# Performance work log

Measured on AMD Instinct MI355X. Metric: run time of the kernel, lower is better.

The kernel has to match this reference:

```python
import jax, jax.numpy as jnp
import numpy as np

N_NODES = 100000


def gcn_conv(h, src, dst, n_nodes):
    """One GCNConv propagation with self-loops and symmetric normalization.
    h: [N, D] already linearly transformed node features.
    src, dst: [E2] int32/int64 edge endpoints (self-loops already appended).
    """
    deg = jnp.zeros((n_nodes,), h.dtype).at[dst].add(jnp.ones_like(dst, dtype=h.dtype))
    dinv = jnp.where(deg > 0, jax.lax.rsqrt(deg), 0.0)  # deg^{-1/2}, 0 for isolated
    norm = dinv[src] * dinv[dst]                         # [E2]
    msgs = norm[:, None] * h[src]                        # gather + scale
    return jnp.zeros((n_nodes, h.shape[1]), h.dtype).at[dst].add(msgs)


def setup_inputs() -> dict:
    key = jax.random.key(0)
    k1, k2, k3, k4 = jax.random.split(key, 4)
    F_IN, HID, N_CLS, N_EDGES = 512, 16, 64, 3200000
    x = jax.random.normal(k1, (N_NODES, F_IN), dtype=jnp.float32)
    edge_index = jax.random.randint(k2, (2, N_EDGES), 0, N_NODES, dtype=jnp.int64)
    W1 = jax.random.normal(k3, (F_IN, HID), dtype=jnp.float32) * (1.0 / np.sqrt(F_IN))
    b1 = jnp.zeros((HID,), jnp.float32)
    W2 = jax.random.normal(k4, (HID, N_CLS), dtype=jnp.float32) * (1.0 / np.sqrt(HID))
    b2 = jnp.zeros((N_CLS,), jnp.float32)
    return {"x": x, "edge_index": edge_index, "W1": W1, "b1": b1, "W2": W2, "b2": b2}


def reference(x, edge_index, W1, b1, W2, b2):
    n = x.shape[0]
    loops = jnp.arange(n, dtype=edge_index.dtype)
    src = jnp.concatenate([edge_index[0], loops])
    dst = jnp.concatenate([edge_index[1], loops])
    # layer 1: transform -> propagate -> bias -> relu (dropout is identity in eval)
    h = gcn_conv(x @ W1, src, dst, n) + b1
    h = jax.nn.relu(h)
    # layer 2
    out = gcn_conv(h @ W2, src, dst, n) + b2
    return out
```

## Files before the change

### kernel.cpp

```cpp
#include <hip/hip_runtime.h>

typedef unsigned short u16;
typedef unsigned int u32;

#define FIN 512
#define HID 16
#define NCLS 64

typedef __bf16 bf16x8 __attribute__((ext_vector_type(8)));
typedef float f32x4 __attribute__((ext_vector_type(4)));

__device__ __forceinline__ float bf2f_raw(u16 u) {
    u32 x = ((u32)u) << 16;
    float f; __builtin_memcpy(&f, &x, 4); return f;
}
__device__ __forceinline__ float ldf(const void* p, long long i, int f32) {
    return f32 ? ((const float*)p)[i] : bf2f_raw(((const u16*)p)[i]);
}
__device__ __forceinline__ u16 f2bf_rne(float v) {
    u32 bits; __builtin_memcpy(&bits, &v, 4);
    u32 lsb = (bits >> 16) & 1;
    bits += 0x7FFFu + lsb;
    return (u16)(bits >> 16);
}

__global__ void k_probe(const void* x, const void* w1, const int* eidx, int E,
                        int* flags) {
    __shared__ int nz_x, nz_w, weird_x, weird_w, odd_nz;
    if (threadIdx.x == 0) { nz_x = 0; nz_w = 0; weird_x = 0; weird_w = 0; odd_nz = 0; }
    __syncthreads();
    const u16* xu = (const u16*)x;
    const u16* wu = (const u16*)w1;
    for (int i = threadIdx.x; i < 8192; i += 256) {
        u16 u = xu[i];
        if (u) atomicOr(&nz_x, 1);
        int e = (u >> 7) & 0xff;
        if ((e == 0 && (u & 0x7f)) || e >= 0xC0) atomicAdd(&weird_x, 1);
        u16 w = wu[i];
        if (w) atomicOr(&nz_w, 1);
        int ew = (w >> 7) & 0xff;
        if ((ew == 0 && (w & 0x7f)) || ew >= 0xC0) atomicAdd(&weird_w, 1);
    }
    int lim = (2 * E < 4096) ? 2 * E : 4096;
    for (int i = 1 + 2 * (int)threadIdx.x; i < lim; i += 512) {
        if (eidx[i] != 0) atomicOr(&odd_nz, 1);
    }
    __syncthreads();
    if (threadIdx.x == 0) {
        flags[0] = (odd_nz == 0) ? 1 : 0;
        flags[1] = (weird_x > 64) ? 1 : 0;
        flags[2] = (weird_w > 64) ? 1 : 0;
        flags[3] = (nz_x == 0) ? 1 : 0;
        flags[4] = (nz_w == 0) ? 1 : 0;
    }
}

__device__ __forceinline__ int ld_src(const int* eidx, int E, int e, int f64) {
    return f64 ? eidx[2LL * e] : eidx[e];
}
__device__ __forceinline__ int ld_dst(const int* eidx, int E, int e, int f64) {
    return f64 ? eidx[2LL * E + 2LL * e] : eidx[(long long)E + e];
}

__global__ void k_count(const int* eidx, const int* flags, int* deg, int E, int n) {
    int e = blockIdx.x * 256 + threadIdx.x;
    if (e >= E) return;
    int d = ld_dst(eidx, E, e, flags[0]);
    if ((unsigned)d < (unsigned)n) atomicAdd(&deg[d], 1);
}

__global__ void k_dinv(const int* deg, float* dinv, int n) {
    int i = blockIdx.x * 256 + threadIdx.x;
    if (i < n) dinv[i] = rsqrtf((float)deg[i] + 1.0f);
}

__global__ void k_scan1(const int* deg, int* part, int n) {
    __shared__ int sd[256];
    int i = blockIdx.x * 256 + threadIdx.x;
    sd[threadIdx.x] = (i < n) ? deg[i] : 0;
    __syncthreads();
    for (int s = 128; s > 0; s >>= 1) {
        if (threadIdx.x < s) sd[threadIdx.x] += sd[threadIdx.x + s];
        __syncthreads();
    }
    if (threadIdx.x == 0) part[blockIdx.x] = sd[0];
}

__global__ void k_scan2(int* part, int nparts, int* row_start, int n) {
    if (nparts > 1024) {
        if (threadIdx.x == 0) {
            int acc = 0;
            for (int b = 0; b < nparts; b++) { int v = part[b]; part[b] = acc; acc += v; }
            row_start[n] = acc;
        }
        return;
    }
    __shared__ int sd[1024];
    int t = threadIdx.x;
    int v = (t < nparts) ? part[t] : 0;
    sd[t] = v;
    __syncthreads();
    for (int s = 1; s < 1024; s <<= 1) {
        int u = (t >= s) ? sd[t - s] : 0;
        __syncthreads();
        sd[t] += u;
        __syncthreads();
    }
    if (t < nparts) part[t] = sd[t] - v;
    if (t == 0) row_start[n] = sd[1023];
}

__global__ void k_scan3(const int* deg, const int* part, int* row_start,
                        int* cursor, int n) {
    __shared__ int sd[256];
    int i = blockIdx.x * 256 + threadIdx.x;
    int v = (i < n) ? deg[i] : 0;
    sd[threadIdx.x] = v;
    __syncthreads();
    for (int s = 1; s < 256; s <<= 1) {
        int u = (threadIdx.x >= s) ? sd[threadIdx.x - s] : 0;
        __syncthreads();
        sd[threadIdx.x] += u;
        __syncthreads();
    }
    if (i < n) {
        int ex = sd[threadIdx.x] - v + part[blockIdx.x];
        row_start[i] = ex;
        cursor[i] = ex;
    }
}

__global__ void k_fill(const int* eidx, const int* flags, int* cursor, int* csr,
                       int E, int n, int nchunk) {
    int r = blockIdx.x & 7;
    int cblk = blockIdx.x >> 3;
    int lo = (int)(((long long)r * n) >> 3);
    int hi = (int)(((long long)(r + 1) * n) >> 3);
    int f64 = flags[0];
    long long stride = (long long)nchunk * 256;
    for (long long e = (long long)cblk * 256 + threadIdx.x; e < E; e += stride) {
        int d = ld_dst(eidx, E, (int)e, f64);
        if (d < lo || d >= hi) continue;
        int s = ld_src(eidx, E, (int)e, f64);
        int slot = atomicAdd(&cursor[d], 1);
        csr[slot] = ((unsigned)s < (unsigned)n) ? s : -1;
    }
}

__global__ void __launch_bounds__(256)
k_gemm1(const void* x, const void* w1, const int* flags, const float* dinv,
        float* h0s, int n) {
    __shared__ __attribute__((aligned(16))) u16 w1t[16 * 512];
    int tid = threadIdx.x;
    int fx = flags[1], fw = flags[2];
    for (int i = tid; i < 8192; i += 256) {
        int k = i >> 4, f = i & 15;
        float v = ldf(w1, (long long)k * HID + f, fw);
        int idx = ((f << 9) + k) ^ ((f & 7) << 3);
        w1t[idx] = f2bf_rne(v);
    }
    __syncthreads();

    int wave = tid >> 6;
    int lane = tid & 63;
    int base = blockIdx.x * 64 + wave * 16;
    if (base >= n) return;
    int rowA = base + (lane & 15);
    if (rowA >= n) rowA = n - 1;
    int g = lane >> 4;
    int nn = lane & 15;
    f32x4 acc = {0.0f, 0.0f, 0.0f, 0.0f};

    if (!fx) {
        const u16* xp = (const u16*)x + (long long)rowA * FIN + g * 8;
        #pragma unroll
        for (int kb = 0; kb < FIN; kb += 32) {
            bf16x8 a = *(const bf16x8*)(xp + kb);
            int bidx = ((nn << 9) + kb + g * 8) ^ ((nn & 7) << 3);
            bf16x8 b = *(const bf16x8*)(w1t + bidx);
            acc = __builtin_amdgcn_mfma_f32_16x16x32_bf16(a, b, acc, 0, 0, 0);
        }
    } else {
        const float* xp = (const float*)x + (long long)rowA * FIN + g * 8;
        #pragma unroll 4
        for (int kb = 0; kb < FIN; kb += 32) {
            float vf[8];
            *(float4*)(vf) = *(const float4*)(xp + kb);
            *(float4*)(vf + 4) = *(const float4*)(xp + kb + 4);
            bf16x8 a;
            #pragma unroll
            for (int j = 0; j < 8; j++) ((u16*)&a)[j] = f2bf_rne(vf[j]);
            int bidx = ((nn << 9) + kb + g * 8) ^ ((nn & 7) << 3);
            bf16x8 b = *(const bf16x8*)(w1t + bidx);
            acc = __builtin_amdgcn_mfma_f32_16x16x32_bf16(a, b, acc, 0, 0, 0);
        }
    }
    #pragma unroll
    for (int r = 0; r < 4; r++) {
        int node = base + g * 4 + r;
        if (node < n) h0s[node * HID + nn] = acc[r] * dinv[node];
    }
}

template <int RELU>
__global__ void k_gather(const int* row_start, const int* csr, const float* dinv,
                         const float* h_in, const void* b, const int* flags,
                         float* h_out, int n) {
    int t = blockIdx.x * 256 + threadIdx.x;
    if (t >= n * 4) return;
    int d = t >> 2;
    int g = t & 3;
    int beg = row_start[d], end = row_start[d + 1];
    const float4* hv = (const float4*)h_in;
    float4 acc = hv[d * 4 + g];
    #pragma unroll 4
    for (int i = beg; i < end; i++) {
        int s = csr[i];
        if (s >= 0) {
            float4 v = hv[s * 4 + g];
            acc.x += v.x; acc.y += v.y; acc.z += v.z; acc.w += v.w;
        }
    }
    float di = dinv[d];
    float4 o;
    if (RELU) {
        int fw = flags[2];
        o.x = di * fmaxf(di * acc.x + ldf(b, g * 4 + 0, fw), 0.0f);
        o.y = di * fmaxf(di * acc.y + ldf(b, g * 4 + 1, fw), 0.0f);
        o.z = di * fmaxf(di * acc.z + ldf(b, g * 4 + 2, fw), 0.0f);
        o.w = di * fmaxf(di * acc.w + ldf(b, g * 4 + 3, fw), 0.0f);
    } else {
        o.x = di * acc.x; o.y = di * acc.y; o.z = di * acc.z; o.w = di * acc.w;
    }
    ((float4*)h_out)[t] = o;
}

__global__ void k_check(const int* eidx, const float* h0s, const float* g,
                        int* flags, int E, int n) {
    __shared__ int h0nz, gnz, dstz;
    if (threadIdx.x == 0) { h0nz = 0; gnz = 0; dstz = 0; }
    __syncthreads();
    for (int i = threadIdx.x; i < 4096; i += 256) {
        if (h0s[i] != 0.0f) atomicOr(&h0nz, 1);
        if (g[i] != 0.0f) atomicOr(&gnz, 1);
    }
    int f64 = flags[0];
    for (int e = threadIdx.x; e < 2048; e += 256) {
        if (ld_dst(eidx, E, e, f64) == 0) atomicAdd(&dstz, 1);
    }
    __syncthreads();
    if (threadIdx.x == 0) {
        int b0 = flags[3];
        int b1 = flags[4];
        int b2 = (dstz > 102);
        int b3 = (h0nz == 0);
        int b4 = (gnz == 0);
        int b5 = flags[1];
        int b6 = flags[2];
        int b7 = flags[0];
        flags[9] = b0 | (b1 << 1) | (b2 << 2) | (b3 << 3) | (b4 << 4) |
                   (b5 << 5) | (b6 << 6) | (b7 << 7);
        flags[8] = (b0 | b1 | b2 | b3 | b4) ? 1 : 0;
    }
}

__global__ void SimplifiedGCN_5574867550498_kernel(
        const float* g, const void* w2, const void* b2, const int* flags,
        float* out, int n) {
    int t = blockIdx.x * 256 + threadIdx.x;
    if (t >= n * NCLS) return;
    int node = t >> 6;
    int c = t & 63;
    int fw = flags[2];
    float acc = ldf(b2, c, fw);
    for (int k = 0; k < HID; k++) {
        acc += g[node * HID + k] * ldf(w2, (long long)k * NCLS + c, fw);
    }
    if (t == 0 && flags[8]) acc = 4096.0f + 2.0f * (float)flags[9];
    out[t] = acc;
}

extern "C" void kernel_launch(void* const* d_in, const int* in_sizes, int n_in,
                              void* d_out, int out_size, void* d_ws, size_t ws_size,
                              hipStream_t stream) {
    const void* x = d_in[0];
    const int* eidx = (const int*)d_in[1];
    const void* w1 = d_in[2];
    const void* b1 = d_in[3];
    const void* w2 = d_in[4];
    const void* b2 = d_in[5];
    float* out = (float*)d_out;

    int n = in_sizes[0] / FIN;
    int E = in_sizes[1] / 2;
    int total_out = n * NCLS;
    int nb_out = (total_out + 255) / 256;
    size_t out_bytes = (size_t)total_out * 4;

    hipMemsetAsync(d_out, 0x42, out_bytes, stream);

    if (n <= 0 || E <= 0 || n_in < 6) {
        hipMemsetAsync(d_out, 0x4E, out_bytes, stream);
        return;
    }

    int nb_n = (n + 255) / 256;
    int nparts = nb_n;

    size_t A = 255;
    size_t o_flags = 0;
    size_t o_deg   = 256;
    size_t o_dinv  = o_deg   + (((size_t)n * 4 + A) & ~A);
    size_t o_rs    = o_dinv  + (((size_t)n * 4 + A) & ~A);
    size_t o_part  = o_rs    + (((size_t)(n + 1) * 4 + A) & ~A);
    size_t o_cur   = o_part  + (((size_t)nparts * 4 + A) & ~A);
    size_t o_h0s   = o_cur   + (((size_t)n * 4 + A) & ~A);
    size_t o_h2ps  = o_h0s   + (((size_t)n * HID * 4 + A) & ~A);
    size_t o_g     = o_h2ps  + (((size_t)n * HID * 4 + A) & ~A);
    size_t o_csr   = o_g     + (((size_t)n * HID * 4 + A) & ~A);
    size_t need    = o_csr   + (((size_t)E * 4 + A) & ~A);

    if (ws_size < need) {
        hipMemsetAsync(d_out, 0x4A, out_bytes, stream);
        return;
    }

    char* p = (char*)d_ws;
    int* flags      = (int*)(p + o_flags);
    int* deg        = (int*)(p + o_deg);
    float* dinv     = (float*)(p + o_dinv);
    int* row_start  = (int*)(p + o_rs);
    int* part       = (int*)(p + o_part);
    int* cursor     = (int*)(p + o_cur);
    float* h0s      = (float*)(p + o_h0s);
    float* h2ps     = (float*)(p + o_h2ps);
    float* g        = (float*)(p + o_g);
    int* csr        = (int*)(p + o_csr);

    int nb_e = (E + 255) / 256;
    int nb_g1 = (n + 63) / 64;
    int nb_h4 = (n * 4 + 255) / 256;
    int nchunk = 256;

    k_probe<<<1, 256, 0, stream>>>(x, w1, eidx, E, flags);
    hipMemsetAsync(deg, 0, (size_t)n * 4, stream);
    k_count<<<nb_e, 256, 0, stream>>>(eidx, flags, deg, E, n);
    k_dinv<<<nb_n, 256, 0, stream>>>(deg, dinv, n);
    k_scan1<<<nb_n, 256, 0, stream>>>(deg, part, n);
    k_scan2<<<1, 1024, 0, stream>>>(part, nparts, row_start, n);
    k_scan3<<<nb_n, 256, 0, stream>>>(deg, part, row_start, cursor, n);
    k_fill<<<nchunk * 8, 256, 0, stream>>>(eidx, flags, cursor, csr, E, n, nchunk);
    k_gemm1<<<nb_g1, 256, 0, stream>>>(x, w1, flags, dinv, h0s, n);
    k_gather<1><<<nb_h4, 256, 0, stream>>>(row_start, csr, dinv, h0s, b1, flags,
                                           h2ps, n);
    k_gather<0><<<nb_h4, 256, 0, stream>>>(row_start, csr, dinv, h2ps, b1, flags,
                                           g, n);
    k_check<<<1, 256, 0, stream>>>(eidx, h0s, g, flags, E, n);
    SimplifiedGCN_5574867550498_kernel<<<nb_out, 256, 0, stream>>>(
        g, w2, b2, flags, out, n);
}
```

Baseline: 775.6 us.

## Replace per-node CSR build with coarse bucket binning and LDS-atomic aggregation

Drops the exact per-node CSR construction (degree count, three-pass scan, range-filtered fill). Edges are instead binned into buckets of 128 destination nodes, each bucket split into 8 sub-cursors to spread the atomic contention, with the destination's local index packed into the upper bits of the source word. Degrees and both aggregation passes then work per bucket, accumulating into shared memory with float atomics, which removes the per-node global atomics and the scan chain. In exchange, the order of the float sums is no longer fixed, LDS atomic contention grows on busy buckets, and node counts are capped at 2^25.

After: 1.270 ms. +63.7%, slower.

```diff
diff --git a/kernel.cpp b/kernel.cpp
--- a/kernel.cpp
+++ b/kernel.cpp
@@ -6,6 +6,10 @@
 #define FIN 512
 #define HID 16
 #define NCLS 64
+
+#define NBSH 7
+#define BUCK (1 << NBSH)
+#define SENTS ((1u << 25) - 1u)
 
 typedef __bf16 bf16x8 __attribute__((ext_vector_type(8)));
 typedef float f32x4 __attribute__((ext_vector_type(4)));
@@ -62,88 +66,85 @@
     return f64 ? eidx[2LL * E + 2LL * e] : eidx[(long long)E + e];
 }
 
-__global__ void k_count(const int* eidx, const int* flags, int* deg, int E, int n) {
-    int e = blockIdx.x * 256 + threadIdx.x;
-    if (e >= E) return;
-    int d = ld_dst(eidx, E, e, flags[0]);
-    if ((unsigned)d < (unsigned)n) atomicAdd(&deg[d], 1);
-}
-
-__global__ void k_dinv(const int* deg, float* dinv, int n) {
-    int i = blockIdx.x * 256 + threadIdx.x;
-    if (i < n) dinv[i] = rsqrtf((float)deg[i] + 1.0f);
-}
-
-__global__ void k_scan1(const int* deg, int* part, int n) {
-    __shared__ int sd[256];
-    int i = blockIdx.x * 256 + threadIdx.x;
-    sd[threadIdx.x] = (i < n) ? deg[i] : 0;
-    __syncthreads();
-    for (int s = 128; s > 0; s >>= 1) {
-        if (threadIdx.x < s) sd[threadIdx.x] += sd[threadIdx.x + s];
+__global__ void k_binA(const int* eidx, const int* flags, int* bcnt8,
+                       int E, int n, int nbuck, int nblocks) {
+    extern __shared__ int lcnt[];
+    int tid = threadIdx.x;
+    for (int i = tid; i < nbuck; i += 256) lcnt[i] = 0;
+    __syncthreads();
+    int f64 = flags[0];
+    long long stride = (long long)nblocks * 256;
+    for (long long e = (long long)blockIdx.x * 256 + tid; e < E; e += stride) {
+        int d = ld_dst(eidx, E, (int)e, f64);
+        if ((unsigned)d < (unsigned)n) atomicAdd(&lcnt[d >> NBSH], 1);
+    }
+    __syncthreads();
+    int sub = blockIdx.x & 7;
+    for (int i = tid; i < nbuck; i += 256) {
+        int v = lcnt[i];
+        if (v) atomicAdd(&bcnt8[i * 8 + sub], v);
+    }
+}
+
+__global__ void k_scanb(const int* bcnt8, int* boff, int* cursor8, int NSUB) {
+    __shared__ int part[1024];
+    int t = threadIdx.x;
+    int K = (NSUB + 1023) >> 10;
+    long long base = (long long)t * K;
+    int local = 0;
+    for (int j = 0; j < K; j++) {
+        long long idx = base + j;
+        if (idx < NSUB) local += bcnt8[idx];
+    }
+    part[t] = local;
+    __syncthreads();
+    for (int s = 1; s < 1024; s <<= 1) {
+        int u = (t >= s) ? part[t - s] : 0;
         __syncthreads();
-    }
-    if (threadIdx.x == 0) part[blockIdx.x] = sd[0];
-}
-
-__global__ void k_scan2(int* part, int nparts, int* row_start, int n) {
-    if (nparts > 1024) {
-        if (threadIdx.x == 0) {
-            int acc = 0;
-            for (int b = 0; b < nparts; b++) { int v = part[b]; part[b] = acc; acc += v; }
-            row_start[n] = acc;
+        part[t] += u;
+        __syncthreads();
+    }
+    int acc = part[t] - local;
+    for (int j = 0; j < K; j++) {
+        long long idx = base + j;
+        if (idx < NSUB) {
+            int v = bcnt8[idx];
+            boff[idx] = acc;
+            cursor8[idx] = acc;
+            acc += v;
         }
-        return;
-    }
-    __shared__ int sd[1024];
-    int t = threadIdx.x;
-    int v = (t < nparts) ? part[t] : 0;
-    sd[t] = v;
-    __syncthreads();
-    for (int s = 1; s < 1024; s <<= 1) {
-        int u = (t >= s) ? sd[t - s] : 0;
-        __syncthreads();
-        sd[t] += u;
-        __syncthreads();
-    }
-    if (t < nparts) part[t] = sd[t] - v;
-    if (t == 0) row_start[n] = sd[1023];
-}
-
-__global__ void k_scan3(const int* deg, const int* part, int* row_start,
-                        int* cursor, int n) {
-    __shared__ int sd[256];
-    int i = blockIdx.x * 256 + threadIdx.x;
-    int v = (i < n) ? deg[i] : 0;
-    sd[threadIdx.x] = v;
-    __syncthreads();
-    for (int s = 1; s < 256; s <<= 1) {
-        int u = (threadIdx.x >= s) ? sd[threadIdx.x - s] : 0;
-        __syncthreads();
-        sd[threadIdx.x] += u;
-        __syncthreads();
-    }
-    if (i < n) {
-        int ex = sd[threadIdx.x] - v + part[blockIdx.x];
-        row_start[i] = ex;
-        cursor[i] = ex;
-    }
-}
-
-__global__ void k_fill(const int* eidx, const int* flags, int* cursor, int* csr,
-                       int E, int n, int nchunk) {
-    int r = blockIdx.x & 7;
-    int cblk = blockIdx.x >> 3;
-    int lo = (int)(((long long)r * n) >> 3);
-    int hi = (int)(((long long)(r + 1) * n) >> 3);
+    }
+    if (t == 1023) boff[NSUB] = part[1023];
+}
+
+__global__ void k_binB(const int* eidx, const int* flags, int* cursor8,
+                       u32* pairs, int E, int n, int nblocks) {
     int f64 = flags[0];
-    long long stride = (long long)nchunk * 256;
-    for (long long e = (long long)cblk * 256 + threadIdx.x; e < E; e += stride) {
+    int sub = blockIdx.x & 7;
+    long long stride = (long long)nblocks * 256;
+    for (long long e = (long long)blockIdx.x * 256 + threadIdx.x; e < E; e += stride) {
         int d = ld_dst(eidx, E, (int)e, f64);
-        if (d < lo || d >= hi) continue;
+        if ((unsigned)d >= (unsigned)n) continue;
         int s = ld_src(eidx, E, (int)e, f64);
-        int slot = atomicAdd(&cursor[d], 1);
-        csr[slot] = ((unsigned)s < (unsigned)n) ? s : -1;
+        u32 su = ((unsigned)s < (unsigned)n) ? (u32)s : SENTS;
+        int slot = atomicAdd(&cursor8[(d >> NBSH) * 8 + sub], 1);
+        pairs[slot] = ((u32)(d & (BUCK - 1)) << 25) | su;
+    }
+}
+
+__global__ void k_dinvC(const u32* pairs, const int* boff, float* dinv,
+                        int n, int nbuck) {
+    __shared__ int cnt[BUCK];
+    int b = blockIdx.x, tid = threadIdx.x;
+    for (int i = tid; i < BUCK; i += 256) cnt[i] = 0;
+    __syncthreads();
+    int beg = boff[b * 8], end = boff[b * 8 + 8];
+    for (int i = beg + tid; i < end; i += 256) atomicAdd(&cnt[pairs[i] >> 25], 1);
+    __syncthreads();
+    int base = b << NBSH;
+    for (int i = tid; i < BUCK; i += 256) {
+        int node = base + i;
+        if (node < n) dinv[node] = rsqrtf((float)cnt[i] + 1.0f);
     }
 }
 
@@ -203,36 +204,50 @@
 }
 
 template <int RELU>
-__global__ void k_gather(const int* row_start, const int* csr, const float* dinv,
-                         const float* h_in, const void* b, const int* flags,
-                         float* h_out, int n) {
-    int t = blockIdx.x * 256 + threadIdx.x;
-    if (t >= n * 4) return;
-    int d = t >> 2;
-    int g = t & 3;
-    int beg = row_start[d], end = row_start[d + 1];
-    const float4* hv = (const float4*)h_in;
-    float4 acc = hv[d * 4 + g];
-    #pragma unroll 4
-    for (int i = beg; i < end; i++) {
-        int s = csr[i];
-        if (s >= 0) {
-            float4 v = hv[s * 4 + g];
-            acc.x += v.x; acc.y += v.y; acc.z += v.z; acc.w += v.w;
+__global__ void __launch_bounds__(256)
+k_gatherL(const u32* pairs, const int* boff, const float* dinv,
+          const float* h_in, const void* bptr, const int* flags,
+          float* h_out, int n) {
+    __shared__ float acc[BUCK * 17];
+    int b = blockIdx.x, tid = threadIdx.x;
+    for (int i = tid; i < BUCK * 17; i += 256) acc[i] = 0.0f;
+    __syncthreads();
+    int beg = boff[b * 8], end = boff[b * 8 + 8];
+    int q = tid & 3;
+    for (int i = beg + (tid >> 2); i < end; i += 64) {
+        u32 pr = pairs[i];
+        u32 s = pr & SENTS;
+        if (s >= (unsigned)n) continue;
+        int dl = pr >> 25;
+        const float4 v = *(const float4*)(h_in + (size_t)s * HID + q * 4);
+        float* a = &acc[dl * 17 + q * 4];
+        atomicAdd(a + 0, v.x);
+        atomicAdd(a + 1, v.y);
+        atomicAdd(a + 2, v.z);
+        atomicAdd(a + 3, v.w);
+    }
+    __syncthreads();
+    int fw = flags[2];
+    int base = b << NBSH;
+    for (int i = tid; i < BUCK * 4; i += 256) {
+        int dl = i >> 2, qq = i & 3;
+        int node = base + dl;
+        if (node >= n) continue;
+        float di = dinv[node];
+        float4 sl = *(const float4*)(h_in + (size_t)node * HID + qq * 4);
+        float* a = &acc[dl * 17 + qq * 4];
+        float ax = a[0] + sl.x, ay = a[1] + sl.y, az = a[2] + sl.z, aw = a[3] + sl.w;
+        float4 o;
+        if (RELU) {
+            o.x = di * fmaxf(di * ax + ldf(bptr, qq * 4 + 0, fw), 0.0f);
+            o.y = di * fmaxf(di * ay + ldf(bptr, qq * 4 + 1, fw), 0.0f);
+            o.z = di * fmaxf(di * az + ldf(bptr, qq * 4 + 2, fw), 0.0f);
+            o.w = di * fmaxf(di * aw + ldf(bptr, qq * 4 + 3, fw), 0.0f);
+        } else {
+            o.x = di * ax; o.y = di * ay; o.z = di * az; o.w = di * aw;
         }
-    }
-    float di = dinv[d];
-    float4 o;
-    if (RELU) {
-        int fw = flags[2];
-        o.x = di * fmaxf(di * acc.x + ldf(b, g * 4 + 0, fw), 0.0f);
-        o.y = di * fmaxf(di * acc.y + ldf(b, g * 4 + 1, fw), 0.0f);
-        o.z = di * fmaxf(di * acc.z + ldf(b, g * 4 + 2, fw), 0.0f);
-        o.w = di * fmaxf(di * acc.w + ldf(b, g * 4 + 3, fw), 0.0f);
-    } else {
-        o.x = di * acc.x; o.y = di * acc.y; o.z = di * acc.z; o.w = di * acc.w;
-    }
-    ((float4*)h_out)[t] = o;
+        *(float4*)(h_out + (size_t)node * HID + qq * 4) = o;
+    }
 }
 
 __global__ void k_check(const int* eidx, const float* h0s, const float* g,
@@ -303,22 +318,25 @@
         hipMemsetAsync(d_out, 0x4E, out_bytes, stream);
         return;
     }
-
-    int nb_n = (n + 255) / 256;
-    int nparts = nb_n;
+    if (n >= (1 << 25)) {
+        hipMemsetAsync(d_out, 0x4B, out_bytes, stream);
+        return;
+    }
+
+    int nbuck = (n + BUCK - 1) >> NBSH;
+    int NSUB = nbuck * 8;
 
     size_t A = 255;
     size_t o_flags = 0;
-    size_t o_deg   = 256;
-    size_t o_dinv  = o_deg   + (((size_t)n * 4 + A) & ~A);
-    size_t o_rs    = o_dinv  + (((size_t)n * 4 + A) & ~A);
-    size_t o_part  = o_rs    + (((size_t)(n + 1) * 4 + A) & ~A);
-    size_t o_cur   = o_part  + (((size_t)nparts * 4 + A) & ~A);
-    size_t o_h0s   = o_cur   + (((size_t)n * 4 + A) & ~A);
-    size_t o_h2ps  = o_h0s   + (((size_t)n * HID * 4 + A) & ~A);
-    size_t o_g     = o_h2ps  + (((size_t)n * HID * 4 + A) & ~A);
-    size_t o_csr   = o_g     + (((size_t)n * HID * 4 + A) & ~A);
-    size_t need    = o_csr   + (((size_t)E * 4 + A) & ~A);
+    size_t o_dinv  = 256;
+    size_t o_h0s   = o_dinv + (((size_t)n * 4 + A) & ~A);
+    size_t o_h2ps  = o_h0s  + (((size_t)n * HID * 4 + A) & ~A);
+    size_t o_g     = o_h2ps + (((size_t)n * HID * 4 + A) & ~A);
+    size_t o_bcnt  = o_g    + (((size_t)n * HID * 4 + A) & ~A);
+    size_t o_boff  = o_bcnt + (((size_t)NSUB * 4 + A) & ~A);
+    size_t o_cur   = o_boff + (((size_t)(NSUB + 1) * 4 + A) & ~A);
+    size_t o_pairs = o_cur  + (((size_t)NSUB * 4 + A) & ~A);
+    size_t need    = o_pairs + (((size_t)E * 4 + A) & ~A);
 
     if (ws_size < need) {
         hipMemsetAsync(d_out, 0x4A, out_bytes, stream);
@@ -326,35 +344,31 @@
     }
 
     char* p = (char*)d_ws;
-    int* flags      = (int*)(p + o_flags);
-    int* deg        = (int*)(p + o_deg);
-    float* dinv     = (float*)(p + o_dinv);
-    int* row_start  = (int*)(p + o_rs);
-    int* part       = (int*)(p + o_part);
-    int* cursor     = (int*)(p + o_cur);
-    float* h0s      = (float*)(p + o_h0s);
-    float* h2ps     = (float*)(p + o_h2ps);
-    float* g        = (float*)(p + o_g);
-    int* csr        = (int*)(p + o_csr);
-
-    int nb_e = (E + 255) / 256;
+    int* flags   = (int*)(p + o_flags);
+    float* dinv  = (float*)(p + o_dinv);
+    float* h0s   = (float*)(p + o_h0s);
+    float* h2ps  = (float*)(p + o_h2ps);
+    float* g     = (float*)(p + o_g);
+    int* bcnt8   = (int*)(p + o_bcnt);
+    int* boff    = (int*)(p + o_boff);
+    int* cursor8 = (int*)(p + o_cur);
+    u32* pairs   = (u32*)(p + o_pairs);
+
     int nb_g1 = (n + 63) / 64;
-    int nb_h4 = (n * 4 + 255) / 256;
-    int nchunk = 256;
+    int nbA = 512, nbB = 1024;
 
     k_probe<<<1, 256, 0, stream>>>(x, w1, eidx, E, flags);
-    hipMemsetAsync(deg, 0, (size_t)n * 4, stream);
-    k_count<<<nb_e, 256, 0, stream>>>(eidx, flags, deg, E, n);
-    k_dinv<<<nb_n, 256, 0, stream>>>(deg, dinv, n);
-    k_scan1<<<nb_n, 256, 0, stream>>>(deg, part, n);
-    k_scan2<<<1, 1024, 0, stream>>>(part, nparts, row_start, n);
-    k_scan3<<<nb_n, 256, 0, stream>>>(deg, part, row_start, cursor, n);
-    k_fill<<<nchunk * 8, 256, 0, stream>>>(eidx, flags, cursor, csr, E, n, nchunk);
+    hipMemsetAsync(bcnt8, 0, (size_t)NSUB * 4, stream);
+    k_binA<<<nbA, 256, (size_t)nbuck * 4, stream>>>(eidx, flags, bcnt8, E, n,
+                                                    nbuck, nbA);
+    k_scanb<<<1, 1024, 0, stream>>>(bcnt8, boff, cursor8, NSUB);
+    k_binB<<<nbB, 256, 0, stream>>>(eidx, flags, cursor8, pairs, E, n, nbB);
+    k_dinvC<<<nbuck, 256, 0, stream>>>(pairs, boff, dinv, n, nbuck);
     k_gemm1<<<nb_g1, 256, 0, stream>>>(x, w1, flags, dinv, h0s, n);
-    k_gather<1><<<nb_h4, 256, 0, stream>>>(row_start, csr, dinv, h0s, b1, flags,
-                                           h2ps, n);
-    k_gather<0><<<nb_h4, 256, 0, stream>>>(row_start, csr, dinv, h2ps, b1, flags,
-                                           g, n);
+    k_gatherL<1><<<nbuck, 256, 0, stream>>>(pairs, boff, dinv, h0s, b1, flags,
+                                            h2ps, n);
+    k_gatherL<0><<<nbuck, 256, 0, stream>>>(pairs, boff, dinv, h2ps, b1, flags,
+                                            g, n);
     k_check<<<1, 256, 0, stream>>>(eidx, h0s, g, flags, E, n);
     SimplifiedGCN_5574867550498_kernel<<<nb_out, 256, 0, stream>>>(
         g, w2, b2, flags, out, n);
```
